# Optimization experiments

Hardware: AMD Instinct MI355X
Metric: run time of the kernel (lower is better)

## Reference

```python
import jax, jax.numpy as jnp
import numpy as np

B, T, D = 4096, 64, 256       # expressions, max tokens per expression, encoding dim
N_SYM, N_OCC = 20000, 131072  # symbols, symbol occurrences


def setup_inputs() -> dict:
    key = jax.random.key(0)
    k1, k2, k3, k4, k5 = jax.random.split(key, 5)
    # unique flattened occurrence positions -> deterministic scatter
    rng = np.random.default_rng(0)
    flat_pos = rng.permutation(B * T)[:N_OCC].astype(np.int64)
    return {
        "expressions_encodings": jax.random.normal(k1, (B, T, D), dtype=jnp.float32),
        "symbols_encodings": jax.random.normal(k2, (N_SYM, D), dtype=jnp.float32),
        "Wf": jax.random.normal(k3, (D, 2 * D), dtype=jnp.float32) * 0.05,
        "bf": jnp.zeros((D,), dtype=jnp.float32),
        "Wa": jax.random.normal(k4, (D, 2 * D), dtype=jnp.float32) * 0.05,
        "ba": jnp.zeros((D,), dtype=jnp.float32),
        "expr_idx": jnp.asarray(flat_pos // T),
        "token_idx": jnp.asarray(flat_pos % T),
        "symbol_idx": jax.random.randint(k5, (N_OCC,), 0, N_SYM, dtype=jnp.int64),
    }


def reference(expressions_encodings, symbols_encodings, Wf, bf, Wa, ba,
              expr_idx, token_idx, symbol_idx):
    b, t, d = expressions_encodings.shape
    flat = expressions_encodings.reshape(b * t, d)            # [B*T, D]
    occ_pos = t * expr_idx + token_idx                        # [N_OCC]
    prev = flat[occ_pos]                                      # gather: [N_OCC, D]
    upd = symbols_encodings[symbol_idx]                       # gather: [N_OCC, D]
    concat = jnp.concatenate([prev, upd], axis=-1)            # [N_OCC, 2D]
    forget = jax.nn.sigmoid(concat @ Wf.T + bf)               # forget gate
    add = jax.nn.sigmoid(concat @ Wa.T + ba)                  # add gate
    new_occ = forget * prev + add * upd                       # gated update
    out = flat.at[occ_pos].set(new_occ)                       # scatter back
    return out.reshape(b, t, d)
```

## Files before the change

### kernel.cpp

```cpp
#include <hip/hip_runtime.h>

typedef __attribute__((ext_vector_type(8))) short short8;
typedef __attribute__((ext_vector_type(4))) short short4v;
typedef __attribute__((ext_vector_type(4))) float floatx4;

__device__ __forceinline__ unsigned short f2bf(float f) {
    unsigned int u = __float_as_uint(f);
    u += 0x7FFFu + ((u >> 16) & 1u);
    return (unsigned short)(u >> 16);
}
__device__ __forceinline__ float bf2f(unsigned short s) {
    return __uint_as_float(((unsigned int)s) << 16);
}

__global__ __launch_bounds__(256)
void convert_w_kernel(const float* __restrict__ Wf,
                      const float* __restrict__ Wa,
                      short* __restrict__ wswz)
{
    int id = blockIdx.x * 256 + threadIdx.x;
    int slot = id & 63;
    int ks   = (id >> 6) & 15;
    int g    = id >> 10;
    int l15  = slot & 15, lk = slot >> 4;
    const float* base = (g < 16) ? (Wf + (long)(g * 16 + l15) * 512)
                                 : (Wa + (long)((g - 16) * 16 + l15) * 512);
    const float* src = base + ks * 32 + lk * 8;
    floatx4 w0 = *(const floatx4*)src;
    floatx4 w1 = *(const floatx4*)(src + 4);
    short8 o;
    o[0] = (short)f2bf(w0[0]); o[1] = (short)f2bf(w0[1]);
    o[2] = (short)f2bf(w0[2]); o[3] = (short)f2bf(w0[3]);
    o[4] = (short)f2bf(w1[0]); o[5] = (short)f2bf(w1[1]);
    o[6] = (short)f2bf(w1[2]); o[7] = (short)f2bf(w1[3]);
    *(short8*)(wswz + (long)id * 8) = o;
}

__global__ __launch_bounds__(256)
void mark_kernel(const int* __restrict__ ei, const int* __restrict__ ti,
                 unsigned char* __restrict__ flags, int n)
{
    int i = blockIdx.x * 256 + threadIdx.x;
    if (i < n) flags[64 * ei[i] + ti[i]] = 1;
}

__global__ __launch_bounds__(256)
void copy_rest_kernel(const float* __restrict__ flat,
                      const unsigned char* __restrict__ flags,
                      float* __restrict__ out, int nrows)
{
    const int lane = threadIdx.x & 63;
    const int w0   = (blockIdx.x * 256 + threadIdx.x) >> 6;
    const int nw   = (gridDim.x * 256) >> 6;
    for (int row = w0; row < nrows; row += nw) {
        if (flags[row]) continue;
        const floatx4* s = (const floatx4*)(flat + (long)row * 256);
        floatx4*       o = (floatx4*)(out + (long)row * 256);
        o[lane] = s[lane];
    }
}

__global__ __launch_bounds__(256, 4)
void gate_gemm_kernel(const float* __restrict__ flat,
                      const float* __restrict__ syms,
                      const float* __restrict__ bfb,
                      const float* __restrict__ bab,
                      const int* __restrict__ expr_idx,
                      const int* __restrict__ token_idx,
                      const int* __restrict__ sym_idx,
                      const short* __restrict__ wswz,
                      float* __restrict__ out)
{
    __shared__ __align__(16) short A_lds[32][520];
    __shared__ int rowbuf[32];
    __shared__ int symbuf[32];

    const int tid  = threadIdx.x;
    const int occ0 = blockIdx.x * 32;

    if (tid < 32) {
        int occ = occ0 + tid;
        rowbuf[tid] = 64 * expr_idx[occ] + token_idx[occ];
        symbuf[tid] = sym_idx[occ];
    }
    __syncthreads();

    {
        const int srow0 = tid >> 4;
        const int se    = tid & 15;
        #pragma unroll
        for (int half = 0; half < 2; ++half) {
            const int srow = srow0 + half * 16;
            const float* prow = flat + (long)rowbuf[srow] * 256;
            const float* urow = syms + (long)symbuf[srow] * 256;
            #pragma unroll
            for (int it = 0; it < 4; ++it) {
                const int k = (se + it * 16) * 4;
                floatx4 v = *(const floatx4*)(prow + k);
                short4v sv;
                sv[0] = (short)f2bf(v[0]); sv[1] = (short)f2bf(v[1]);
                sv[2] = (short)f2bf(v[2]); sv[3] = (short)f2bf(v[3]);
                *(short4v*)&A_lds[srow][k] = sv;
            }
            #pragma unroll
            for (int it = 0; it < 4; ++it) {
                const int k = (se + it * 16) * 4;
                floatx4 v = *(const floatx4*)(urow + k);
                short4v sv;
                sv[0] = (short)f2bf(v[0]); sv[1] = (short)f2bf(v[1]);
                sv[2] = (short)f2bf(v[2]); sv[3] = (short)f2bf(v[3]);
                *(short4v*)&A_lds[srow][256 + k] = sv;
            }
        }
    }
    __syncthreads();

    const int lane  = tid & 63;
    const int wv    = tid >> 6;
    const int l15   = lane & 15;
    const int lk    = lane >> 4;
    const int dbase = wv * 64;

    floatx4 acc[2][8];
    #pragma unroll
    for (int r = 0; r < 2; ++r)
        #pragma unroll
        for (int c = 0; c < 8; ++c)
            acc[r][c] = (floatx4){0.f, 0.f, 0.f, 0.f};

    const short8* wsv = (const short8*)wswz;

    #pragma unroll
    for (int ks = 0; ks < 16; ++ks) {
        short8 af0 = *(const short8*)&A_lds[l15][ks * 32 + lk * 8];
        short8 af1 = *(const short8*)&A_lds[16 + l15][ks * 32 + lk * 8];
        #pragma unroll
        for (int c = 0; c < 8; ++c) {
            const int g = (c < 4) ? (wv * 4 + c) : (16 + wv * 4 + (c - 4));
            short8 bfr = wsv[(g * 16 + ks) * 64 + lk * 16 + l15];
            acc[0][c] = __builtin_amdgcn_mfma_f32_16x16x32_bf16(af0, bfr, acc[0][c], 0, 0, 0);
            acc[1][c] = __builtin_amdgcn_mfma_f32_16x16x32_bf16(af1, bfr, acc[1][c], 0, 0, 0);
        }
    }

    float bfv[4], bav[4];
    #pragma unroll
    for (int cf = 0; cf < 4; ++cf) {
        const int d = dbase + cf * 16 + l15;
        bfv[cf] = bfb[d];
        bav[cf] = bab[d];
    }

    #pragma unroll
    for (int r = 0; r < 2; ++r) {
        #pragma unroll
        for (int j = 0; j < 4; ++j) {
            const int ml = r * 16 + lk * 4 + j;
            float* orow = out + (long)rowbuf[ml] * 256;
            #pragma unroll
            for (int cf = 0; cf < 4; ++cf) {
                const int d = dbase + cf * 16 + l15;
                float prev = bf2f((unsigned short)A_lds[ml][d]);
                float upd  = bf2f((unsigned short)A_lds[ml][256 + d]);
                float fg = 1.f / (1.f + __expf(-(acc[r][cf][j]     + bfv[cf])));
                float ag = 1.f / (1.f + __expf(-(acc[r][4 + cf][j] + bav[cf])));
                orow[d] = fg * prev + ag * upd;
            }
        }
    }
}

extern "C" void kernel_launch(void* const* d_in, const int* in_sizes, int n_in,
                              void* d_out, int out_size, void* d_ws, size_t ws_size,
                              hipStream_t stream) {
    const float* flat = (const float*)d_in[0];
    const float* syms = (const float*)d_in[1];
    const float* Wf   = (const float*)d_in[2];
    const float* bf   = (const float*)d_in[3];
    const float* Wa   = (const float*)d_in[4];
    const float* ba   = (const float*)d_in[5];
    const int* ei     = (const int*)d_in[6];
    const int* ti     = (const int*)d_in[7];
    const int* si     = (const int*)d_in[8];
    float* out        = (float*)d_out;

    short* wswz          = (short*)d_ws;
    unsigned char* flags = (unsigned char*)d_ws + 512 * 1024;

    const int n_occ = in_sizes[6];
    const int nrows = out_size / 256;

    hipMemsetAsync(flags, 0, nrows, stream);
    mark_kernel<<<(n_occ + 255) / 256, 256, 0, stream>>>(ei, ti, flags, n_occ);

    convert_w_kernel<<<128, 256, 0, stream>>>(Wf, Wa, wswz);

    gate_gemm_kernel<<<n_occ / 32, 256, 0, stream>>>(flat, syms, bf, ba,
                                                     ei, ti, si, wswz, out);

    copy_rest_kernel<<<2048, 256, 0, stream>>>(flat, flags, out, nrows);
}
```

Before: 229.4 us.

## Use 64-occurrence tiles with 8 waves and swapped MFMA operands for vector stores

```diff
diff --git a/kernel.cpp b/kernel.cpp
--- a/kernel.cpp
+++ b/kernel.cpp
@@ -11,6 +11,9 @@
 }
 __device__ __forceinline__ float bf2f(unsigned short s) {
     return __uint_as_float(((unsigned int)s) << 16);
+}
+__device__ __forceinline__ float sigmoidf(float x) {
+    return 1.f / (1.f + __expf(-x));
 }
 
 __global__ __launch_bounds__(256)
@@ -60,7 +63,7 @@
     }
 }
 
-__global__ __launch_bounds__(256, 4)
+__global__ __launch_bounds__(512, 4)
 void gate_gemm_kernel(const float* __restrict__ flat,
                       const float* __restrict__ syms,
                       const float* __restrict__ bfb,
@@ -71,14 +74,14 @@
                       const short* __restrict__ wswz,
                       float* __restrict__ out)
 {
-    __shared__ __align__(16) short A_lds[32][520];
-    __shared__ int rowbuf[32];
-    __shared__ int symbuf[32];
+    __shared__ __align__(16) short A_lds[64][520];
+    __shared__ int rowbuf[64];
+    __shared__ int symbuf[64];
 
     const int tid  = threadIdx.x;
-    const int occ0 = blockIdx.x * 32;
-
-    if (tid < 32) {
+    const int occ0 = blockIdx.x * 64;
+
+    if (tid < 64) {
         int occ = occ0 + tid;
         rowbuf[tid] = 64 * expr_idx[occ] + token_idx[occ];
         symbuf[tid] = sym_idx[occ];
@@ -86,86 +89,82 @@
     __syncthreads();
 
     {
-        const int srow0 = tid >> 4;
-        const int se    = tid & 15;
-        #pragma unroll
-        for (int half = 0; half < 2; ++half) {
-            const int srow = srow0 + half * 16;
-            const float* prow = flat + (long)rowbuf[srow] * 256;
-            const float* urow = syms + (long)symbuf[srow] * 256;
-            #pragma unroll
-            for (int it = 0; it < 4; ++it) {
-                const int k = (se + it * 16) * 4;
-                floatx4 v = *(const floatx4*)(prow + k);
-                short4v sv;
-                sv[0] = (short)f2bf(v[0]); sv[1] = (short)f2bf(v[1]);
-                sv[2] = (short)f2bf(v[2]); sv[3] = (short)f2bf(v[3]);
-                *(short4v*)&A_lds[srow][k] = sv;
-            }
-            #pragma unroll
-            for (int it = 0; it < 4; ++it) {
-                const int k = (se + it * 16) * 4;
-                floatx4 v = *(const floatx4*)(urow + k);
-                short4v sv;
-                sv[0] = (short)f2bf(v[0]); sv[1] = (short)f2bf(v[1]);
-                sv[2] = (short)f2bf(v[2]); sv[3] = (short)f2bf(v[3]);
-                *(short4v*)&A_lds[srow][256 + k] = sv;
-            }
+        const int srow = tid >> 3;
+        const int se   = tid & 7;
+        const float* prow = flat + (long)rowbuf[srow] * 256;
+        const float* urow = syms + (long)symbuf[srow] * 256;
+        #pragma unroll
+        for (int it = 0; it < 8; ++it) {
+            const int k = (se + it * 8) * 4;
+            floatx4 v = *(const floatx4*)(prow + k);
+            short4v sv;
+            sv[0] = (short)f2bf(v[0]); sv[1] = (short)f2bf(v[1]);
+            sv[2] = (short)f2bf(v[2]); sv[3] = (short)f2bf(v[3]);
+            *(short4v*)&A_lds[srow][k] = sv;
+        }
+        #pragma unroll
+        for (int it = 0; it < 8; ++it) {
+            const int k = (se + it * 8) * 4;
+            floatx4 v = *(const floatx4*)(urow + k);
+            short4v sv;
+            sv[0] = (short)f2bf(v[0]); sv[1] = (short)f2bf(v[1]);
+            sv[2] = (short)f2bf(v[2]); sv[3] = (short)f2bf(v[3]);
+            *(short4v*)&A_lds[srow][256 + k] = sv;
         }
     }
     __syncthreads();
 
-    const int lane  = tid & 63;
-    const int wv    = tid >> 6;
-    const int l15   = lane & 15;
-    const int lk    = lane >> 4;
-    const int dbase = wv * 64;
-
-    floatx4 acc[2][8];
+    const int lane = tid & 63;
+    const int wv   = tid >> 6;
+    const int l15  = lane & 15;
+    const int lk   = lane >> 4;
+
+    floatx4 acc[4][4];
     #pragma unroll
-    for (int r = 0; r < 2; ++r)
-        #pragma unroll
-        for (int c = 0; c < 8; ++c)
-            acc[r][c] = (floatx4){0.f, 0.f, 0.f, 0.f};
+    for (int mi = 0; mi < 4; ++mi)
+        #pragma unroll
+        for (int c = 0; c < 4; ++c)
+            acc[mi][c] = (floatx4){0.f, 0.f, 0.f, 0.f};
 
     const short8* wsv = (const short8*)wswz;
 
     #pragma unroll
     for (int ks = 0; ks < 16; ++ks) {
-        short8 af0 = *(const short8*)&A_lds[l15][ks * 32 + lk * 8];
-        short8 af1 = *(const short8*)&A_lds[16 + l15][ks * 32 + lk * 8];
-        #pragma unroll
-        for (int c = 0; c < 8; ++c) {
-            const int g = (c < 4) ? (wv * 4 + c) : (16 + wv * 4 + (c - 4));
-            short8 bfr = wsv[(g * 16 + ks) * 64 + lk * 16 + l15];
-            acc[0][c] = __builtin_amdgcn_mfma_f32_16x16x32_bf16(af0, bfr, acc[0][c], 0, 0, 0);
-            acc[1][c] = __builtin_amdgcn_mfma_f32_16x16x32_bf16(af1, bfr, acc[1][c], 0, 0, 0);
-        }
-    }
-
-    float bfv[4], bav[4];
+        short8 cb[4];
+        #pragma unroll
+        for (int mi = 0; mi < 4; ++mi)
+            cb[mi] = *(const short8*)&A_lds[mi * 16 + l15][ks * 32 + lk * 8];
+
+        #pragma unroll
+        for (int c = 0; c < 4; ++c) {
+            const int g = (c < 2) ? (wv * 2 + c) : (16 + wv * 2 + (c - 2));
+            short8 wf = wsv[(g * 16 + ks) * 64 + lane];
+            #pragma unroll
+            for (int mi = 0; mi < 4; ++mi)
+                acc[mi][c] = __builtin_amdgcn_mfma_f32_16x16x32_bf16(
+                    wf, cb[mi], acc[mi][c], 0, 0, 0);
+        }
+    }
+
     #pragma unroll
-    for (int cf = 0; cf < 4; ++cf) {
-        const int d = dbase + cf * 16 + l15;
-        bfv[cf] = bfb[d];
-        bav[cf] = bab[d];
-    }
-
-    #pragma unroll
-    for (int r = 0; r < 2; ++r) {
-        #pragma unroll
-        for (int j = 0; j < 4; ++j) {
-            const int ml = r * 16 + lk * 4 + j;
-            float* orow = out + (long)rowbuf[ml] * 256;
+    for (int c = 0; c < 2; ++c) {
+        const int d0 = wv * 32 + c * 16 + lk * 4;
+        const floatx4 bfv = *(const floatx4*)(bfb + d0);
+        const floatx4 bav = *(const floatx4*)(bab + d0);
+        #pragma unroll
+        for (int mi = 0; mi < 4; ++mi) {
+            const int m = mi * 16 + l15;
+            short4v pv = *(const short4v*)&A_lds[m][d0];
+            short4v uv = *(const short4v*)&A_lds[m][256 + d0];
+            floatx4 res;
             #pragma unroll
-            for (int cf = 0; cf < 4; ++cf) {
-                const int d = dbase + cf * 16 + l15;
-                float prev = bf2f((unsigned short)A_lds[ml][d]);
-                float upd  = bf2f((unsigned short)A_lds[ml][256 + d]);
-                float fg = 1.f / (1.f + __expf(-(acc[r][cf][j]     + bfv[cf])));
-                float ag = 1.f / (1.f + __expf(-(acc[r][4 + cf][j] + bav[cf])));
-                orow[d] = fg * prev + ag * upd;
+            for (int j = 0; j < 4; ++j) {
+                float fg = sigmoidf(acc[mi][c][j]     + bfv[j]);
+                float ag = sigmoidf(acc[mi][c + 2][j] + bav[j]);
+                res[j] = fg * bf2f((unsigned short)pv[j])
+                       + ag * bf2f((unsigned short)uv[j]);
             }
+            *(floatx4*)(out + (long)rowbuf[m] * 256 + d0) = res;
         }
     }
 }
@@ -195,7 +194,7 @@
 
     convert_w_kernel<<<128, 256, 0, stream>>>(Wf, Wa, wswz);
 
-    gate_gemm_kernel<<<n_occ / 32, 256, 0, stream>>>(flat, syms, bf, ba,
+    gate_gemm_kernel<<<n_occ / 64, 512, 0, stream>>>(flat, syms, bf, ba,
                                                      ei, ti, si, wswz, out);
 
     copy_rest_kernel<<<2048, 256, 0, stream>>>(flat, flags, out, nrows);
```

Result: slower. 241.5 us (+5.3%).
